# Performance work log

Measured on AMD Instinct MI355X. Metric: run time of the kernel, lower is better.

## Reference

```python
import jax, jax.numpy as jnp
import numpy as np
from jax import lax

B, A, T, D, V, K = 16, 1024, 512, 256, 50000, 3
EXP_DILS = [1, 2, 4, 8, 16, 32, 32]  # conv_num=7, exp_num=5
REF_DILS = [1, 1, 1]                 # refine_num=3


def setup_inputs() -> dict:
    key = jax.random.key(0)
    ks = jax.random.split(key, 14)
    inp = {
        'article_word': jax.random.randint(ks[0], (B, A), 0, V),
        'article_char': jax.random.randint(ks[1], (B, A, 16), 0, 100),
        'template_word': jax.random.randint(ks[2], (B, T), 0, V),
        'template_char': jax.random.randint(ks[3], (B, T, 16), 0, 100),
        'article_mask': jnp.ones((B, A), jnp.float32),
        'template_mask': jnp.ones((B, T), jnp.float32),
        'emb': jax.random.normal(ks[4], (V, D), jnp.float32) * 0.02,
        'exp_w': jax.random.normal(ks[5], (7, K, D, 2 * D), jnp.float32) * 0.03,
        'exp_b': jnp.zeros((7, 2 * D), jnp.float32),
        'ref_w': jax.random.normal(ks[6], (3, K, D, 2 * D), jnp.float32) * 0.03,
        'ref_b': jnp.zeros((3, 2 * D), jnp.float32),
        'ff1_w': jax.random.normal(ks[7], (10, 10), jnp.float32) * 0.3,
        'ff1_b': jnp.zeros((10,), jnp.float32),
        'ff2_w': jax.random.normal(ks[8], (10, 1), jnp.float32) * 0.3,
        'ff2_b': jnp.zeros((1,), jnp.float32),
    }
    return inp


def _res_block(x, w, b, dilation):
    # x: [B, L, D]; w: [K, D, 2D]  (Conv1d, padding='same' given k//2*dilation)
    pad = (K // 2) * dilation
    y = lax.conv_general_dilated(x, w, window_strides=(1,), padding=[(pad, pad)],
                                 rhs_dilation=(dilation,),
                                 dimension_numbers=('NWC', 'WIO', 'NWC')) + b
    a, g = jnp.split(y, 2, axis=2)  # GLU on channel dim
    return x + a * jax.nn.sigmoid(g)


def _encode(x, exp_w, exp_b, ref_w, ref_b):
    for i, d in enumerate(EXP_DILS):
        x = _res_block(x, exp_w[i], exp_b[i], d)
    for i, d in enumerate(REF_DILS):
        x = _res_block(x, ref_w[i], ref_b[i], d)
    return x  # dropout is identity in eval mode


def reference(article_word, article_char, template_word, template_char,
              article_mask, template_mask, emb, exp_w, exp_b, ref_w, ref_b,
              ff1_w, ff1_b, ff2_w, ff2_b):
    art = _encode(emb[article_word], exp_w, exp_b, ref_w, ref_b)    # [B,A,D]
    tpl = _encode(emb[template_word], exp_w, exp_b, ref_w, ref_b)   # [B,T,D]
    # pairwise squared distance without materializing [B,A,T,D]
    a2 = jnp.sum(art * art, axis=-1)                 # [B,A]
    t2 = jnp.sum(tpl * tpl, axis=-1)                 # [B,T]
    dot = jnp.einsum('bad,btd->bat', art, tpl)       # [B,A,T]
    dist = jnp.maximum(a2[:, :, None] + t2[:, None, :] - 2.0 * dot, 0.0)
    S = jnp.exp(-dist) * article_mask[:, :, None] * template_mask[:, None, :]
    row_max = jnp.max(S, axis=2)                     # [B,A]
    top, _ = lax.top_k(row_max, 10)                  # sorted descending, [B,10]
    h = jax.nn.relu(top @ ff1_w + ff1_b)             # [B,10]
    out = (h @ ff2_w + ff2_b).squeeze()              # [B]
    return out
```

## Files before the change

kernel.cpp:

```cpp
#include <hip/hip_runtime.h>
#include <math.h>

#define NB 16
#define NA 1024
#define NT 512
#define ND 256
#define PAD 32

typedef short bf8_t __attribute__((ext_vector_type(8)));
typedef float f4_t __attribute__((ext_vector_type(4)));

__device__ __forceinline__ float bf2f(ushort u) {
    union { unsigned int i; float f; } v; v.i = ((unsigned int)u) << 16; return v.f;
}
__device__ __forceinline__ ushort f2bf(float f) {
    union { float f; unsigned int i; } v; v.f = f;
    unsigned int x = v.i;
    unsigned int r = (x + 0x7fffu + ((x >> 16) & 1u)) >> 16;
    return (ushort)r;
}
__device__ __forceinline__ void gl_lds16(const void* g, void* l) {
    __builtin_amdgcn_global_load_lds(
        (const __attribute__((address_space(1))) unsigned int*)g,
        (__attribute__((address_space(3))) unsigned int*)l, 16, 0, 0);
}


__global__ void pad_zero(ushort* __restrict__ art_a, ushort* __restrict__ art_b,
                         ushort* __restrict__ tpl_a, ushort* __restrict__ tpl_b) {
    int y = blockIdx.y;
    ushort* p = (y == 0) ? art_a : (y == 1) ? art_b : (y == 2) ? tpl_a : tpl_b;
    int L = (y < 2) ? NA : NT;
    int Lp = L + 2 * PAD;
    int idx = blockIdx.x * 256 + threadIdx.x;
    int plane = idx >> 6;
    int row_in = idx & 63;
    int slab = (row_in < PAD) ? row_in : L + row_in;
    uint4 z = make_uint4(0, 0, 0, 0);
    *(uint4*)(p + ((size_t)plane * Lp + slab) * 8) = z;
}

__global__ void gather_emb_bf16(const int* __restrict__ words,
                                const float* __restrict__ emb,
                                ushort* __restrict__ out, int Lbits, int Lp, int n) {
    int idx = blockIdx.x * 256 + threadIdx.x;
    if (idx >= n) return;
    int L = 1 << Lbits;
    int l = idx & (L - 1);
    int bq = idx >> Lbits;
    int qq = bq & 31, b = bq >> 5;
    int wd = words[b * L + l];
    const float4* src = (const float4*)(emb + (size_t)wd * ND + qq * 8);
    float4 v0 = src[0], v1 = src[1];
    ushort o[8];
    o[0]=f2bf(v0.x); o[1]=f2bf(v0.y); o[2]=f2bf(v0.z); o[3]=f2bf(v0.w);
    o[4]=f2bf(v1.x); o[5]=f2bf(v1.y); o[6]=f2bf(v1.z); o[7]=f2bf(v1.w);
    *(uint4*)(out + ((size_t)bq * Lp + PAD + l) * 8) = *(uint4*)o;
}

__global__ void __launch_bounds__(256)
repack_w(const float* __restrict__ exp_w, const float* __restrict__ ref_w,
         ushort* __restrict__ wpack) {
    __shared__ float tile[64][65];
    int li = blockIdx.z;
    int gk = blockIdx.x;
    int gc = blockIdx.y;
    const float* src = (li < 7) ? exp_w + (size_t)li * 3 * ND * 512
                                : ref_w + (size_t)(li - 7) * 3 * ND * 512;
    int k0g = gk * 64, c0 = gc * 64;
    int tid = threadIdx.x;
    #pragma unroll
    for (int p = 0; p < 4; ++p) {
        int kr = p * 16 + (tid >> 4);
        int cc = (tid & 15) * 4;
        *(float4*)&tile[kr][cc] =
            *(const float4*)(src + (size_t)(k0g + kr) * 512 + c0 + cc);
    }
    __syncthreads();
    int tap = k0g >> 8, kl0 = k0g & 255, kc0 = kl0 >> 5;
    int ag = c0 >> 8, cb = (c0 & 255) >> 6;
    int kg = tid >> 5, idx = tid & 31;
    int kc = kc0 + (kg >> 2), qq = kg & 3;
    #pragma unroll
    for (int h = 0; h < 2; ++h) {
        int w64 = idx + h * 32;
        int cprime = h * 64 + ag * 32 + idx;
        ushort o[8];
        #pragma unroll
        for (int j = 0; j < 8; ++j) o[j] = f2bf(tile[kg * 8 + j][w64]);
        ushort* d = wpack +
            (((((size_t)(li * 4 + cb) * 3 + tap) * 8 + kc) * 4 + qq) * 128 + cprime) * 8;
        *(uint4*)d = *(uint4*)o;
    }
}

__global__ void __launch_bounds__(256, 3)
conv_glu_mfma(const ushort* __restrict__ art_x, ushort* __restrict__ art_y,
              const ushort* __restrict__ tpl_x, ushort* __restrict__ tpl_y,
              const ushort* __restrict__ wp, const float* __restrict__ bias,
              int dil) {
    __shared__ char smem[34816];
    ushort* Als = (ushort*)smem;
    float* ylds = (float*)smem;

    const int tid = threadIdx.x;
    const int w = tid >> 6, lane = tid & 63;
    const int wm = w >> 1, wn = w & 1;
    const int q = lane >> 4, l15 = lane & 15;

    const int id = blockIdx.x;
    const int cb = (id >> 3) & 3;
    const int pb = ((id >> 5) << 3) | (id & 7);
    const int plane = pb % 12;
    const int b = pb / 12;
    const int b32 = b * 32;

    int Lp, l0;
    const ushort* xb;
    ushort* yb;
    if (plane < 8) {
        Lp = NA + 2 * PAD; l0 = plane * 128;
        xb = art_x; yb = art_y;
    } else {
        Lp = NT + 2 * PAD; l0 = (plane - 8) * 128;
        xb = tpl_x; yb = tpl_y;
    }
    const ushort* wl = wp + (size_t)cb * 98304;
    const int boff = (q * 128 + wn * 64 + l15) * 8;

    f4_t acc[4][4];
    #pragma unroll
    for (int i = 0; i < 4; ++i)
        #pragma unroll
        for (int j = 0; j < 4; ++j)
            acc[i][j] = (f4_t){0.f, 0.f, 0.f, 0.f};

    for (int kc2 = 0; kc2 < 4; ++kc2) {
        #pragma unroll
        for (int s3 = 0; s3 < 6; ++s3) {
            int s = w + s3 * 4;
            int h = s / 12, within = s % 12;
            int qq = kc2 * 8 + h * 4 + within / 3;
            int rphys = l0 + (within % 3) * 64 + lane;
            gl_lds16(xb + ((size_t)(b32 + qq) * Lp + rphys) * 8, Als + s * 512);
        }
        __syncthreads();

        #pragma unroll
        for (int h = 0; h < 2; ++h) {
            const int kc = kc2 * 2 + h;
            bf8_t bfr[3][4];
            const ushort* wkc = wl + kc * 4096 + boff;
            #pragma unroll
            for (int t = 0; t < 3; ++t)
                #pragma unroll
                for (int nt = 0; nt < 4; ++nt)
                    bfr[t][nt] = *(const bf8_t*)(wkc + t * 32768 + nt * 128);

            const ushort* Ah = Als + h * 6144;
            #pragma unroll
            for (int t = 0; t < 3; ++t) {
                const int sh = (t - 1) * dil;
                bf8_t af[4];
                #pragma unroll
                for (int mt = 0; mt < 4; ++mt)
                    af[mt] = *(const bf8_t*)(Ah + (q * 192 + 32 + sh + wm * 64 + mt * 16 + l15) * 8);
                #pragma unroll
                for (int mt = 0; mt < 4; ++mt)
                    #pragma unroll
                    for (int nt = 0; nt < 4; ++nt)
                        acc[mt][nt] = __builtin_amdgcn_mfma_f32_16x16x32_bf16(
                            af[mt], bfr[t][nt], acc[mt][nt], 0, 0, 0);
            }
        }
        __syncthreads();
    }

    #pragma unroll
    for (int nt = 0; nt < 2; ++nt) {
        const int cl = wn * 32 + nt * 16 + l15;
        const int chan = cb * 64 + cl;
        const float ba = bias[chan];
        const float bg2 = bias[chan + 256];
        #pragma unroll
        for (int mt = 0; mt < 4; ++mt) {
            #pragma unroll
            for (int r = 0; r < 4; ++r) {
                const int row = wm * 64 + mt * 16 + q * 4 + r;
                float av = acc[mt][nt][r] + ba;
                float gv = acc[mt][nt + 2][r] + bg2;
                ylds[row * 68 + cl] = av / (1.f + __expf(-gv));
            }
        }
    }
    __syncthreads();

    #pragma unroll
    for (int p = 0; p < 4; ++p) {
        int u = p * 256 + tid;
        int cl8 = u >> 7;
        int row = u & 127;
        size_t go = ((size_t)(b32 + cb * 8 + cl8) * Lp + l0 + PAD + row) * 8;
        ushort xv[8]; *(uint4*)xv = *(const uint4*)(xb + go);
        float4 y0 = *(float4*)&ylds[row * 68 + cl8 * 8];
        float4 y1 = *(float4*)&ylds[row * 68 + cl8 * 8 + 4];
        ushort ov[8];
        ov[0]=f2bf(bf2f(xv[0])+y0.x); ov[1]=f2bf(bf2f(xv[1])+y0.y);
        ov[2]=f2bf(bf2f(xv[2])+y0.z); ov[3]=f2bf(bf2f(xv[3])+y0.w);
        ov[4]=f2bf(bf2f(xv[4])+y1.x); ov[5]=f2bf(bf2f(xv[5])+y1.y);
        ov[6]=f2bf(bf2f(xv[6])+y1.z); ov[7]=f2bf(bf2f(xv[7])+y1.w);
        *(uint4*)(yb + go) = *(uint4*)ov;
    }
}

__global__ void sumsq_bf16(const ushort* __restrict__ x, float* __restrict__ out,
                           int L, int Lp) {
    __shared__ float red[4][64];
    int tid = threadIdx.x;
    int r = tid & 63, pg = tid >> 6;
    int row_g = blockIdx.x * 64 + r;
    int b = row_g / L, l = row_g - b * L;
    float s = 0.f;
    #pragma unroll
    for (int j = 0; j < 8; ++j) {
        int qq = pg * 8 + j;
        const ushort* p = x + ((size_t)(b * 32 + qq) * Lp + PAD + l) * 8;
        ushort v[8]; *(uint4*)v = *(const uint4*)p;
        #pragma unroll
        for (int e = 0; e < 8; ++e) { float f = bf2f(v[e]); s += f * f; }
    }
    red[pg][r] = s;
    __syncthreads();
    if (tid < 64)
        out[blockIdx.x * 64 + tid] =
            red[0][tid] + red[1][tid] + red[2][tid] + red[3][tid];
}

__global__ void __launch_bounds__(256)
dist_rowmax_mfma(const ushort* __restrict__ art, const ushort* __restrict__ tpl,
                 const float* __restrict__ a2, const float* __restrict__ t2,
                 const float* __restrict__ amask, const float* __restrict__ tmask,
                 float* __restrict__ rmaxp) {
    __shared__ ushort Als[128 * 32];
    __shared__ ushort Bls[128 * 32];
    __shared__ float red[2][128];

    const int tid = threadIdx.x;
    const int w = tid >> 6, lane = tid & 63;
    const int wm = w >> 1, wn = w & 1;
    const int q = lane >> 4, l15 = lane & 15;

    const int id = blockIdx.x;
    const int b = (id & 7) | (((id >> 3) & 1) << 3);
    const int rest = id >> 4;
    const int a0 = (rest & 7) * 128;
    const int tplane = rest >> 3;
    const int t0 = tplane * 128;
    const int b32 = b * 32;
    const int LpA = NA + 2 * PAD, LpT = NT + 2 * PAD;

    float a2v[4][4], amv[4][4];
    #pragma unroll
    for (int mt = 0; mt < 4; ++mt)
        #pragma unroll
        for (int r = 0; r < 4; ++r) {
            int row = a0 + wm * 64 + mt * 16 + q * 4 + r;
            a2v[mt][r] = a2[b * NA + row];
            amv[mt][r] = amask[b * NA + row];
        }

    f4_t acc[4][4];
    #pragma unroll
    for (int i = 0; i < 4; ++i)
        #pragma unroll
        for (int j = 0; j < 4; ++j)
            acc[i][j] = (f4_t){0.f, 0.f, 0.f, 0.f};

    for (int kb = 0; kb < 8; ++kb) {
        #pragma unroll
        for (int s3 = 0; s3 < 2; ++s3) {
            int s = w + s3 * 4;
            int qq = kb * 4 + (s >> 1);
            int r0 = (s & 1) * 64;
            gl_lds16(art + ((size_t)(b32 + qq) * LpA + PAD + a0 + r0 + lane) * 8,
                     Als + s * 512);
            gl_lds16(tpl + ((size_t)(b32 + qq) * LpT + PAD + t0 + r0 + lane) * 8,
                     Bls + s * 512);
        }
        __syncthreads();

        bf8_t af[4], bfr[4];
        #pragma unroll
        for (int mt = 0; mt < 4; ++mt)
            af[mt] = *(const bf8_t*)(Als + (q * 128 + wm * 64 + mt * 16 + l15) * 8);
        #pragma unroll
        for (int nt = 0; nt < 4; ++nt)
            bfr[nt] = *(const bf8_t*)(Bls + (q * 128 + wn * 64 + nt * 16 + l15) * 8);
        #pragma unroll
        for (int mt = 0; mt < 4; ++mt)
            #pragma unroll
            for (int nt = 0; nt < 4; ++nt)
                acc[mt][nt] = __builtin_amdgcn_mfma_f32_16x16x32_bf16(
                    af[mt], bfr[nt], acc[mt][nt], 0, 0, 0);
        __syncthreads();
    }

    float rm[4][4];
    #pragma unroll
    for (int mt = 0; mt < 4; ++mt)
        #pragma unroll
        for (int r = 0; r < 4; ++r) rm[mt][r] = 0.f;

    #pragma unroll
    for (int nt = 0; nt < 4; ++nt) {
        int t = t0 + wn * 64 + nt * 16 + l15;
        float t2v = t2[b * NT + t];
        float tmv = tmask[b * NT + t];
        #pragma unroll
        for (int mt = 0; mt < 4; ++mt)
            #pragma unroll
            for (int r = 0; r < 4; ++r) {
                float d = a2v[mt][r] + t2v - 2.f * acc[mt][nt][r];
                d = fmaxf(d, 0.f);
                float s = __expf(-d) * amv[mt][r] * tmv;
                rm[mt][r] = fmaxf(rm[mt][r], s);
            }
    }
    #pragma unroll
    for (int mt = 0; mt < 4; ++mt)
        #pragma unroll
        for (int r = 0; r < 4; ++r) {
            float v = rm[mt][r];
            #pragma unroll
            for (int off = 1; off < 16; off <<= 1)
                v = fmaxf(v, __shfl_xor(v, off));
            rm[mt][r] = v;
        }
    if (l15 == 0) {
        #pragma unroll
        for (int mt = 0; mt < 4; ++mt)
            #pragma unroll
            for (int r = 0; r < 4; ++r)
                red[wn][wm * 64 + mt * 16 + q * 4 + r] = rm[mt][r];
    }
    __syncthreads();
    if (tid < 128)
        rmaxp[((size_t)tplane * NB + b) * NA + a0 + tid] =
            fmaxf(red[0][tid], red[1][tid]);
}

__global__ void __launch_bounds__(256)
topk_mlp_kernel(const float* __restrict__ rmaxp,
                const float* __restrict__ ff1_w, const float* __restrict__ ff1_b,
                const float* __restrict__ ff2_w, const float* __restrict__ ff2_b,
                float* __restrict__ out) {
    __shared__ float vals[NA];
    __shared__ float top[10];
    __shared__ float h[10];
    __shared__ float rv[4];
    __shared__ int ri[4];

    int b = blockIdx.x;
    int tid = threadIdx.x;
    int lane = tid & 63, wv = tid >> 6;
    for (int i = tid; i < NA; i += 256) {
        float m = rmaxp[(size_t)b * NA + i];
        m = fmaxf(m, rmaxp[((size_t)NB + b) * NA + i]);
        m = fmaxf(m, rmaxp[((size_t)2 * NB + b) * NA + i]);
        m = fmaxf(m, rmaxp[((size_t)3 * NB + b) * NA + i]);
        vals[i] = m;
    }
    __syncthreads();

    for (int it = 0; it < 10; ++it) {
        float best = -1e30f;
        int bi = 0;
        #pragma unroll
        for (int u = 0; u < 4; ++u) {
            int i = u * 256 + tid;
            if (vals[i] > best) { best = vals[i]; bi = i; }
        }
        #pragma unroll
        for (int off = 32; off; off >>= 1) {
            float ob = __shfl_down(best, off);
            int oi = __shfl_down(bi, off);
            if (ob > best) { best = ob; bi = oi; }
        }
        if (lane == 0) { rv[wv] = best; ri[wv] = bi; }
        __syncthreads();
        if (tid == 0) {
            float bb = rv[0]; int bbi = ri[0];
            #pragma unroll
            for (int k = 1; k < 4; ++k)
                if (rv[k] > bb) { bb = rv[k]; bbi = ri[k]; }
            top[it] = bb; vals[bbi] = -1e30f;
        }
        __syncthreads();
    }

    if (tid < 10) {
        float s = ff1_b[tid];
        #pragma unroll
        for (int i = 0; i < 10; ++i) s += top[i] * ff1_w[i * 10 + tid];
        h[tid] = fmaxf(s, 0.f);
    }
    __syncthreads();
    if (tid == 0) {
        float s = ff2_b[0];
        #pragma unroll
        for (int j = 0; j < 10; ++j) s += h[j] * ff2_w[j];
        out[b] = s;
    }
}

extern "C" void kernel_launch(void* const* d_in, const int* in_sizes, int n_in,
                              void* d_out, int out_size, void* d_ws, size_t ws_size,
                              hipStream_t stream) {
    const int*   art_w = (const int*)d_in[0];
    const int*   tpl_w = (const int*)d_in[2];
    const float* amask = (const float*)d_in[4];
    const float* tmask = (const float*)d_in[5];
    const float* emb   = (const float*)d_in[6];
    const float* exp_w = (const float*)d_in[7];
    const float* exp_b = (const float*)d_in[8];
    const float* ref_w = (const float*)d_in[9];
    const float* ref_b = (const float*)d_in[10];
    const float* ff1_w = (const float*)d_in[11];
    const float* ff1_b = (const float*)d_in[12];
    const float* ff2_w = (const float*)d_in[13];
    const float* ff2_b = (const float*)d_in[14];
    float* out = (float*)d_out;

    const size_t art_bytes = (size_t)NB * 32 * (NA + 2 * PAD) * 8 * 2;
    const size_t tpl_bytes = (size_t)NB * 32 * (NT + 2 * PAD) * 8 * 2;
    const size_t wpk_bytes = (size_t)10 * 4 * 3 * 8 * 4 * 128 * 8 * 2;

    char* p = (char*)d_ws;
    ushort* art_a = (ushort*)p; p += art_bytes;
    ushort* art_b = (ushort*)p; p += art_bytes;
    ushort* tpl_a = (ushort*)p; p += tpl_bytes;
    ushort* tpl_b = (ushort*)p; p += tpl_bytes;
    ushort* wpack = (ushort*)p; p += wpk_bytes;
    float* a2    = (float*)p; p += (size_t)NB * NA * 4;
    float* t2    = (float*)p; p += (size_t)NB * NT * 4;
    float* rmaxp = (float*)p; p += (size_t)4 * NB * NA * 4;

    pad_zero<<<dim3(128, 4), 256, 0, stream>>>(art_a, art_b, tpl_a, tpl_b);
    repack_w<<<dim3(12, 8, 10), 256, 0, stream>>>(exp_w, ref_w, wpack);

    {
        int n = NB * 32 * NA;
        gather_emb_bf16<<<(n + 255) / 256, 256, 0, stream>>>(art_w, emb, art_a, 10, NA + 64, n);
        n = NB * 32 * NT;
        gather_emb_bf16<<<(n + 255) / 256, 256, 0, stream>>>(tpl_w, emb, tpl_a, 9, NT + 64, n);
    }

    const int dils[10] = {1, 2, 4, 8, 16, 32, 32, 1, 1, 1};

    ushort* a_cur = art_a; ushort* a_nxt = art_b;
    ushort* t_cur = tpl_a; ushort* t_nxt = tpl_b;
    for (int i = 0; i < 10; ++i) {
        const ushort* wl = wpack + (size_t)i * 4 * 98304;
        const float* bb = (i < 7) ? exp_b + (size_t)i * 512
                                  : ref_b + (size_t)(i - 7) * 512;
        conv_glu_mfma<<<768, 256, 0, stream>>>(
            a_cur, a_nxt, t_cur, t_nxt, wl, bb, dils[i]);
        ushort* t1 = a_cur; a_cur = a_nxt; a_nxt = t1;
        ushort* t2p = t_cur; t_cur = t_nxt; t_nxt = t2p;
    }
    ushort* art_fin = a_cur;
    ushort* tpl_fin = t_cur;

    sumsq_bf16<<<(NB * NA) / 64, 256, 0, stream>>>(art_fin, a2, NA, NA + 64);
    sumsq_bf16<<<(NB * NT) / 64, 256, 0, stream>>>(tpl_fin, t2, NT, NT + 64);

    dist_rowmax_mfma<<<512, 256, 0, stream>>>(
        art_fin, tpl_fin, a2, t2, amask, tmask, rmaxp);

    topk_mlp_kernel<<<NB, 256, 0, stream>>>(rmaxp, ff1_w, ff1_b, ff2_w, ff2_b, out);
}
```

Measured before the change: 387.0 us.

## Fuse prep and sumsq launches, raise conv occupancy, halve dist tile rows

Merges the padding-zero and two embedding-gather kernels into one prep kernel, and the two sumsq launches into one 2D launch, to cut launch overhead. In the conv kernel, weight fragments are now loaded per tap instead of all three taps up front, and the launch bound is raised from 3 to 4 blocks per SM to lower register pressure and raise occupancy. The distance kernel uses 64-row article tiles instead of 128 and doubles its grid, giving more blocks and fewer registers, at the cost of reloading template tiles more often. Loading weights per tap may expose more global-load latency inside the MFMA loop.

```diff
diff --git a/kernel.cpp b/kernel.cpp
--- a/kernel.cpp
+++ b/kernel.cpp
@@ -26,36 +26,47 @@
 }
 
 
-__global__ void pad_zero(ushort* __restrict__ art_a, ushort* __restrict__ art_b,
-                         ushort* __restrict__ tpl_a, ushort* __restrict__ tpl_b) {
-    int y = blockIdx.y;
-    ushort* p = (y == 0) ? art_a : (y == 1) ? art_b : (y == 2) ? tpl_a : tpl_b;
-    int L = (y < 2) ? NA : NT;
-    int Lp = L + 2 * PAD;
+__global__ void prep_kernel(const int* __restrict__ art_w, const int* __restrict__ tpl_w,
+                            const float* __restrict__ emb,
+                            ushort* __restrict__ art_a, ushort* __restrict__ art_b,
+                            ushort* __restrict__ tpl_a, ushort* __restrict__ tpl_b) {
     int idx = blockIdx.x * 256 + threadIdx.x;
-    int plane = idx >> 6;
-    int row_in = idx & 63;
-    int slab = (row_in < PAD) ? row_in : L + row_in;
-    uint4 z = make_uint4(0, 0, 0, 0);
-    *(uint4*)(p + ((size_t)plane * Lp + slab) * 8) = z;
-}
-
-__global__ void gather_emb_bf16(const int* __restrict__ words,
-                                const float* __restrict__ emb,
-                                ushort* __restrict__ out, int Lbits, int Lp, int n) {
-    int idx = blockIdx.x * 256 + threadIdx.x;
-    if (idx >= n) return;
-    int L = 1 << Lbits;
-    int l = idx & (L - 1);
-    int bq = idx >> Lbits;
-    int qq = bq & 31, b = bq >> 5;
-    int wd = words[b * L + l];
-    const float4* src = (const float4*)(emb + (size_t)wd * ND + qq * 8);
-    float4 v0 = src[0], v1 = src[1];
-    ushort o[8];
-    o[0]=f2bf(v0.x); o[1]=f2bf(v0.y); o[2]=f2bf(v0.z); o[3]=f2bf(v0.w);
-    o[4]=f2bf(v1.x); o[5]=f2bf(v1.y); o[6]=f2bf(v1.z); o[7]=f2bf(v1.w);
-    *(uint4*)(out + ((size_t)bq * Lp + PAD + l) * 8) = *(uint4*)o;
+    if (idx < NB * 32 * NA) {
+        int l = idx & (NA - 1);
+        int bq = idx >> 10;
+        int qq = bq & 31, b = bq >> 5;
+        int wd = art_w[b * NA + l];
+        const float4* src = (const float4*)(emb + (size_t)wd * ND + qq * 8);
+        float4 v0 = src[0], v1 = src[1];
+        ushort o[8];
+        o[0]=f2bf(v0.x); o[1]=f2bf(v0.y); o[2]=f2bf(v0.z); o[3]=f2bf(v0.w);
+        o[4]=f2bf(v1.x); o[5]=f2bf(v1.y); o[6]=f2bf(v1.z); o[7]=f2bf(v1.w);
+        *(uint4*)(art_a + ((size_t)bq * (NA + 64) + PAD + l) * 8) = *(uint4*)o;
+    } else if (idx < NB * 32 * NA + NB * 32 * NT) {
+        int j = idx - NB * 32 * NA;
+        int l = j & (NT - 1);
+        int bq = j >> 9;
+        int qq = bq & 31, b = bq >> 5;
+        int wd = tpl_w[b * NT + l];
+        const float4* src = (const float4*)(emb + (size_t)wd * ND + qq * 8);
+        float4 v0 = src[0], v1 = src[1];
+        ushort o[8];
+        o[0]=f2bf(v0.x); o[1]=f2bf(v0.y); o[2]=f2bf(v0.z); o[3]=f2bf(v0.w);
+        o[4]=f2bf(v1.x); o[5]=f2bf(v1.y); o[6]=f2bf(v1.z); o[7]=f2bf(v1.w);
+        *(uint4*)(tpl_a + ((size_t)bq * (NT + 64) + PAD + l) * 8) = *(uint4*)o;
+    } else {
+        int j = idx - (NB * 32 * NA + NB * 32 * NT);
+        int y = j >> 15;
+        int rem = j & 32767;
+        ushort* p = (y == 0) ? art_a : (y == 1) ? art_b : (y == 2) ? tpl_a : tpl_b;
+        int L = (y < 2) ? NA : NT;
+        int Lp = L + 2 * PAD;
+        int plane = rem >> 6;
+        int row_in = rem & 63;
+        int slab = (row_in < PAD) ? row_in : L + row_in;
+        uint4 z = make_uint4(0, 0, 0, 0);
+        *(uint4*)(p + ((size_t)plane * Lp + slab) * 8) = z;
+    }
 }
 
 __global__ void __launch_bounds__(256)
@@ -94,7 +105,7 @@
     }
 }
 
-__global__ void __launch_bounds__(256, 3)
+__global__ void __launch_bounds__(256, 4)
 conv_glu_mfma(const ushort* __restrict__ art_x, ushort* __restrict__ art_y,
               const ushort* __restrict__ tpl_x, ushort* __restrict__ tpl_y,
               const ushort* __restrict__ wp, const float* __restrict__ bias,
@@ -149,17 +160,14 @@
         #pragma unroll
         for (int h = 0; h < 2; ++h) {
             const int kc = kc2 * 2 + h;
-            bf8_t bfr[3][4];
             const ushort* wkc = wl + kc * 4096 + boff;
-            #pragma unroll
-            for (int t = 0; t < 3; ++t)
+            const ushort* Ah = Als + h * 6144;
+            #pragma unroll
+            for (int t = 0; t < 3; ++t) {
+                bf8_t bfr[4];
                 #pragma unroll
                 for (int nt = 0; nt < 4; ++nt)
-                    bfr[t][nt] = *(const bf8_t*)(wkc + t * 32768 + nt * 128);
-
-            const ushort* Ah = Als + h * 6144;
-            #pragma unroll
-            for (int t = 0; t < 3; ++t) {
+                    bfr[nt] = *(const bf8_t*)(wkc + t * 32768 + nt * 128);
                 const int sh = (t - 1) * dil;
                 bf8_t af[4];
                 #pragma unroll
@@ -170,7 +178,7 @@
                     #pragma unroll
                     for (int nt = 0; nt < 4; ++nt)
                         acc[mt][nt] = __builtin_amdgcn_mfma_f32_16x16x32_bf16(
-                            af[mt], bfr[t][nt], acc[mt][nt], 0, 0, 0);
+                            af[mt], bfr[nt], acc[mt][nt], 0, 0, 0);
             }
         }
         __syncthreads();
@@ -213,9 +221,15 @@
     }
 }
 
-__global__ void sumsq_bf16(const ushort* __restrict__ x, float* __restrict__ out,
-                           int L, int Lp) {
+__global__ void sumsq_bf16(const ushort* __restrict__ art, const ushort* __restrict__ tpl,
+                           float* __restrict__ a2, float* __restrict__ t2) {
     __shared__ float red[4][64];
+    int which = blockIdx.y;
+    if (which == 1 && blockIdx.x >= 128) return;
+    const ushort* x = which ? tpl : art;
+    float* out = which ? t2 : a2;
+    int L = which ? NT : NA;
+    int Lp = L + 2 * PAD;
     int tid = threadIdx.x;
     int r = tid & 63, pg = tid >> 6;
     int row_g = blockIdx.x * 64 + r;
@@ -236,14 +250,14 @@
             red[0][tid] + red[1][tid] + red[2][tid] + red[3][tid];
 }
 
-__global__ void __launch_bounds__(256)
+__global__ void __launch_bounds__(256, 4)
 dist_rowmax_mfma(const ushort* __restrict__ art, const ushort* __restrict__ tpl,
                  const float* __restrict__ a2, const float* __restrict__ t2,
                  const float* __restrict__ amask, const float* __restrict__ tmask,
                  float* __restrict__ rmaxp) {
-    __shared__ ushort Als[128 * 32];
+    __shared__ ushort Als[64 * 32];
     __shared__ ushort Bls[128 * 32];
-    __shared__ float red[2][128];
+    __shared__ float red[2][64];
 
     const int tid = threadIdx.x;
     const int w = tid >> 6, lane = tid & 63;
@@ -253,51 +267,56 @@
     const int id = blockIdx.x;
     const int b = (id & 7) | (((id >> 3) & 1) << 3);
     const int rest = id >> 4;
-    const int a0 = (rest & 7) * 128;
-    const int tplane = rest >> 3;
+    const int a0 = (rest & 15) * 64;
+    const int tplane = rest >> 4;
     const int t0 = tplane * 128;
     const int b32 = b * 32;
     const int LpA = NA + 2 * PAD, LpT = NT + 2 * PAD;
 
-    float a2v[4][4], amv[4][4];
-    #pragma unroll
-    for (int mt = 0; mt < 4; ++mt)
+    float a2v[2][4], amv[2][4];
+    #pragma unroll
+    for (int mt = 0; mt < 2; ++mt)
         #pragma unroll
         for (int r = 0; r < 4; ++r) {
-            int row = a0 + wm * 64 + mt * 16 + q * 4 + r;
+            int row = a0 + wm * 32 + mt * 16 + q * 4 + r;
             a2v[mt][r] = a2[b * NA + row];
             amv[mt][r] = amask[b * NA + row];
         }
 
-    f4_t acc[4][4];
-    #pragma unroll
-    for (int i = 0; i < 4; ++i)
+    f4_t acc[2][4];
+    #pragma unroll
+    for (int i = 0; i < 2; ++i)
         #pragma unroll
         for (int j = 0; j < 4; ++j)
             acc[i][j] = (f4_t){0.f, 0.f, 0.f, 0.f};
 
     for (int kb = 0; kb < 8; ++kb) {
         #pragma unroll
-        for (int s3 = 0; s3 < 2; ++s3) {
+        for (int s3 = 0; s3 < 3; ++s3) {
             int s = w + s3 * 4;
-            int qq = kb * 4 + (s >> 1);
-            int r0 = (s & 1) * 64;
-            gl_lds16(art + ((size_t)(b32 + qq) * LpA + PAD + a0 + r0 + lane) * 8,
-                     Als + s * 512);
-            gl_lds16(tpl + ((size_t)(b32 + qq) * LpT + PAD + t0 + r0 + lane) * 8,
-                     Bls + s * 512);
-        }
-        __syncthreads();
-
-        bf8_t af[4], bfr[4];
-        #pragma unroll
-        for (int mt = 0; mt < 4; ++mt)
-            af[mt] = *(const bf8_t*)(Als + (q * 128 + wm * 64 + mt * 16 + l15) * 8);
+            if (s < 4) {
+                int qq = kb * 4 + s;
+                gl_lds16(art + ((size_t)(b32 + qq) * LpA + PAD + a0 + lane) * 8,
+                         Als + s * 512);
+            } else {
+                int s2 = s - 4;
+                int qq = kb * 4 + (s2 >> 1);
+                int r0 = (s2 & 1) * 64;
+                gl_lds16(tpl + ((size_t)(b32 + qq) * LpT + PAD + t0 + r0 + lane) * 8,
+                         Bls + s2 * 512);
+            }
+        }
+        __syncthreads();
+
+        bf8_t af[2], bfr[4];
+        #pragma unroll
+        for (int mt = 0; mt < 2; ++mt)
+            af[mt] = *(const bf8_t*)(Als + (q * 64 + wm * 32 + mt * 16 + l15) * 8);
         #pragma unroll
         for (int nt = 0; nt < 4; ++nt)
             bfr[nt] = *(const bf8_t*)(Bls + (q * 128 + wn * 64 + nt * 16 + l15) * 8);
         #pragma unroll
-        for (int mt = 0; mt < 4; ++mt)
+        for (int mt = 0; mt < 2; ++mt)
             #pragma unroll
             for (int nt = 0; nt < 4; ++nt)
                 acc[mt][nt] = __builtin_amdgcn_mfma_f32_16x16x32_bf16(
@@ -305,9 +324,9 @@
         __syncthreads();
     }
 
-    float rm[4][4];
-    #pragma unroll
-    for (int mt = 0; mt < 4; ++mt)
+    float rm[2][4];
+    #pragma unroll
+    for (int mt = 0; mt < 2; ++mt)
         #pragma unroll
         for (int r = 0; r < 4; ++r) rm[mt][r] = 0.f;
 
@@ -317,7 +336,7 @@
         float t2v = t2[b * NT + t];
         float tmv = tmask[b * NT + t];
         #pragma unroll
-        for (int mt = 0; mt < 4; ++mt)
+        for (int mt = 0; mt < 2; ++mt)
             #pragma unroll
             for (int r = 0; r < 4; ++r) {
                 float d = a2v[mt][r] + t2v - 2.f * acc[mt][nt][r];
@@ -327,7 +346,7 @@
             }
     }
     #pragma unroll
-    for (int mt = 0; mt < 4; ++mt)
+    for (int mt = 0; mt < 2; ++mt)
         #pragma unroll
         for (int r = 0; r < 4; ++r) {
             float v = rm[mt][r];
@@ -338,13 +357,13 @@
         }
     if (l15 == 0) {
         #pragma unroll
-        for (int mt = 0; mt < 4; ++mt)
+        for (int mt = 0; mt < 2; ++mt)
             #pragma unroll
             for (int r = 0; r < 4; ++r)
-                red[wn][wm * 64 + mt * 16 + q * 4 + r] = rm[mt][r];
-    }
-    __syncthreads();
-    if (tid < 128)
+                red[wn][wm * 32 + mt * 16 + q * 4 + r] = rm[mt][r];
+    }
+    __syncthreads();
+    if (tid < 64)
         rmaxp[((size_t)tplane * NB + b) * NA + a0 + tid] =
             fmaxf(red[0][tid], red[1][tid]);
 }
@@ -445,14 +464,11 @@
     float* t2    = (float*)p; p += (size_t)NB * NT * 4;
     float* rmaxp = (float*)p; p += (size_t)4 * NB * NA * 4;
 
-    pad_zero<<<dim3(128, 4), 256, 0, stream>>>(art_a, art_b, tpl_a, tpl_b);
     repack_w<<<dim3(12, 8, 10), 256, 0, stream>>>(exp_w, ref_w, wpack);
-
     {
-        int n = NB * 32 * NA;
-        gather_emb_bf16<<<(n + 255) / 256, 256, 0, stream>>>(art_w, emb, art_a, 10, NA + 64, n);
-        n = NB * 32 * NT;
-        gather_emb_bf16<<<(n + 255) / 256, 256, 0, stream>>>(tpl_w, emb, tpl_a, 9, NT + 64, n);
+        int n = NB * 32 * NA + NB * 32 * NT + 4 * NB * 32 * 64;
+        prep_kernel<<<(n + 255) / 256, 256, 0, stream>>>(
+            art_w, tpl_w, emb, art_a, art_b, tpl_a, tpl_b);
     }
 
     const int dils[10] = {1, 2, 4, 8, 16, 32, 32, 1, 1, 1};
@@ -471,10 +487,9 @@
     ushort* art_fin = a_cur;
     ushort* tpl_fin = t_cur;
 
-    sumsq_bf16<<<(NB * NA) / 64, 256, 0, stream>>>(art_fin, a2, NA, NA + 64);
-    sumsq_bf16<<<(NB * NT) / 64, 256, 0, stream>>>(tpl_fin, t2, NT, NT + 64);
-
-    dist_rowmax_mfma<<<512, 256, 0, stream>>>(
+    sumsq_bf16<<<dim3(256, 2), 256, 0, stream>>>(art_fin, tpl_fin, a2, t2);
+
+    dist_rowmax_mfma<<<1024, 256, 0, stream>>>(
         art_fin, tpl_fin, a2, t2, amask, tmask, rmaxp);
 
     topk_mlp_kernel<<<NB, 256, 0, stream>>>(rmaxp, ff1_w, ff1_b, ff2_w, ff2_b, out);
```

Measured after the change: 382.5 us. Within noise of the previous version (-1.2%).
